# Performance work log

Measured on AMD Instinct MI355X. Metric: run time of the kernel, lower is better.

## Reference

```python
import jax, jax.numpy as jnp
import numpy as np


def _conv1x1_prelu(x, w, b, a):
    # 1x1 conv == channel matmul; PReLU with shared scalar slope a
    y = jnp.einsum('oc,nchw->nohw', w, x) + b[None, :, None, None]
    return jnp.where(y >= 0, y, a * y)


def setup_inputs() -> dict:
    key = jax.random.key(0)
    ks = jax.random.split(key, 7)
    N, C, H, W = 2, 128, 96, 96
    Ce = 64  # channel // reduction
    s_in = 1.0 / np.sqrt(C)
    return {
        'input': jax.random.normal(ks[0], (N, C, H, W), jnp.float32),
        'w1': jax.random.normal(ks[1], (Ce, C), jnp.float32) * s_in,
        'b1': jnp.zeros((Ce,), jnp.float32),
        'a1': jnp.full((1,), 0.25, jnp.float32),
        'w2': jax.random.normal(ks[2], (Ce, C), jnp.float32) * s_in,
        'b2': jnp.zeros((Ce,), jnp.float32),
        'a2': jnp.full((1,), 0.25, jnp.float32),
        'wa': jax.random.normal(ks[3], (C, C), jnp.float32) * s_in,
        'ba': jnp.zeros((C,), jnp.float32),
        'aa': jnp.full((1,), 0.25, jnp.float32),
    }


def reference(input, w1, b1, a1, w2, b2, a2, wa, ba, aa):
    e1 = _conv1x1_prelu(input, w1, b1, a1[0])  # [N, Ce, H, W]
    e2 = _conv1x1_prelu(input, w2, b2, a2[0])  # [N, Ce, H, W]
    xa = _conv1x1_prelu(input, wa, ba, aa[0])  # [N, C,  H, W]
    N, Ce, H, W = e1.shape
    HW = H * W
    q = e1.transpose(0, 2, 3, 1).reshape(N, HW, Ce)   # [N, HW, Ce]
    k = e2.reshape(N, Ce, HW)                          # [N, Ce, HW]
    score = jax.nn.softmax(jnp.matmul(q, k), axis=-1)  # [N, HW, HW] (no scale, as in source)
    v = xa.reshape(N, -1, HW).transpose(0, 2, 1)       # [N, HW, C]
    out = jnp.matmul(score, v)                         # [N, HW, C]
    return out.transpose(0, 2, 1).reshape(N, -1, H, W)
```

## Files before the change

### kernel.cpp

```cpp
#include <hip/hip_runtime.h>
#include <cstdint>
#include <cstddef>

#define HW_ 9216
#define CC 128
#define NQT 144
#define NQT2 72
#define LOG2E 1.44269504088896f

typedef short bf16x8 __attribute__((ext_vector_type(8)));
typedef unsigned short u16x4 __attribute__((ext_vector_type(4)));
typedef unsigned short u16x8 __attribute__((ext_vector_type(8)));
typedef float f32x4 __attribute__((ext_vector_type(4)));

__device__ __forceinline__ unsigned short f2bf(float f) {
    unsigned int u = __builtin_bit_cast(unsigned int, f);
    u += 0x7FFFu + ((u >> 16) & 1u);
    return (unsigned short)(u >> 16);
}

__device__ __forceinline__ float fast_exp2(float x) {
#if __has_builtin(__builtin_amdgcn_exp2f)
    return __builtin_amdgcn_exp2f(x);
#else
    return exp2f(x);
#endif
}

__device__ __forceinline__ unsigned int cvt_pk_bf16(float lo, float hi) {
    unsigned int r;
    asm("v_cvt_pk_bf16_f32 %0, %1, %2" : "=v"(r) : "v"(lo), "v"(hi));
    return r;
}

__global__ __launch_bounds__(256) void prep_w(const float* __restrict__ w1,
                                              const float* __restrict__ w2,
                                              const float* __restrict__ wa,
                                              float* __restrict__ wt) {
    int idx = blockIdx.x * 256 + threadIdx.x;
    int o = idx >> 7, c = idx & 127;
    float v;
    if (o < 64)       v = w1[o * 128 + c];
    else if (o < 128) v = w2[(o - 64) * 128 + c];
    else              v = wa[(o - 128) * 128 + c];
    wt[c * 256 + o] = v;
}

__global__ __launch_bounds__(256) void conv_kernel(
    const float* __restrict__ x, const float* __restrict__ wt,
    const float* __restrict__ b1, const float* __restrict__ a1,
    const float* __restrict__ b2, const float* __restrict__ a2,
    const float* __restrict__ ba, const float* __restrict__ aa,
    unsigned short* __restrict__ qb, unsigned short* __restrict__ kb,
    unsigned short* __restrict__ vtb) {
    const int ptile = blockIdx.x;
    const int oset  = blockIdx.y;
    const int n     = blockIdx.z;
    const int t = threadIdx.x;
    const int p = t & 63;
    const int og = __builtin_amdgcn_readfirstlane(t >> 6);
    const int p0 = ptile * 64;

    __shared__ float xs[128 * 64];
    for (int c = t >> 6; c < 128; c += 4)
        xs[c * 64 + p] = x[((size_t)n * CC + c) * HW_ + p0 + p];
    __syncthreads();

    const int obase = oset * 64 + og * 16;
    float acc[16];
#pragma unroll
    for (int i = 0; i < 16; i++) acc[i] = 0.f;

    for (int c = 0; c < 128; c++) {
        float xv = xs[c * 64 + p];
        const float* wr = wt + c * 256 + obase;
#pragma unroll
        for (int i = 0; i < 16; i++) acc[i] = fmaf(wr[i], xv, acc[i]);
    }

    const float* bias_p;
    const float* slope_p;
    if (oset == 0)      { bias_p = b1; slope_p = a1; }
    else if (oset == 1) { bias_p = b2; slope_p = a2; }
    else                { bias_p = ba; slope_p = aa; }
    const float slope = slope_p[0];

    unsigned short vals[16];
#pragma unroll
    for (int i = 0; i < 16; i++) {
        float bv = (oset < 2) ? bias_p[og * 16 + i] : bias_p[obase - 128 + i];
        float y = acc[i] + bv;
        y = (y >= 0.f) ? y : slope * y;
        if (oset == 0) y *= LOG2E;
        vals[i] = f2bf(y);
    }

    if (oset < 2) {
        unsigned short* dst = (oset == 0 ? qb : kb) + ((size_t)n * HW_ + p0 + p) * 64 + og * 16;
        bf16x8 v0, v1;
#pragma unroll
        for (int i = 0; i < 8; i++) { v0[i] = (short)vals[i]; v1[i] = (short)vals[8 + i]; }
        *(bf16x8*)(dst)     = v0;
        *(bf16x8*)(dst + 8) = v1;
    } else {
        int c0 = obase - 128;
#pragma unroll
        for (int i = 0; i < 16; i++)
            vtb[((size_t)n * CC + c0 + i) * HW_ + p0 + p] = vals[i];
    }
}

__global__ __launch_bounds__(256, 2) void attn_kernel(
    const unsigned short* __restrict__ qb, const unsigned short* __restrict__ kb,
    const unsigned short* __restrict__ vtb,
    float* __restrict__ o_part, float* __restrict__ l_part,
    int nch, int chunk_j) {
    const int qt    = blockIdx.x;
    const int chunk = blockIdx.y;
    const int n     = blockIdx.z;
    const int t = threadIdx.x;
    const int w = t >> 6;
    const int lane = t & 63;
    const int l15 = lane & 15;
    const int quad = lane >> 4;
    const int e7 = l15 & 7;

    __shared__ __align__(16) unsigned short k_lds[64 * 64];
    __shared__ __align__(16) unsigned short v_lds[128 * 64];
    __shared__ __align__(16) unsigned short p_lds[4 * 1024];

    const int row_ga = qt * 128 + w * 32 + l15;
    const int row_gb = row_ga + 16;
    const bf16x8 bq0a = *(const bf16x8*)(qb + ((size_t)n * HW_ + row_ga) * 64 + quad * 8);
    const bf16x8 bq1a = *(const bf16x8*)(qb + ((size_t)n * HW_ + row_ga) * 64 + 32 + quad * 8);
    const bf16x8 bq0b = *(const bf16x8*)(qb + ((size_t)n * HW_ + row_gb) * 64 + quad * 8);
    const bf16x8 bq1b = *(const bf16x8*)(qb + ((size_t)n * HW_ + row_gb) * 64 + 32 + quad * 8);

    f32x4 acc_oa[8], acc_ob[8];
#pragma unroll
    for (int i = 0; i < 8; i++) {
        acc_oa[i] = (f32x4){0.f, 0.f, 0.f, 0.f};
        acc_ob[i] = (f32x4){0.f, 0.f, 0.f, 0.f};
    }
    float l_sa = 0.f, l_sb = 0.f;

    const int stg_row = t >> 3, stg_seg = t & 7;
    const int iters = chunk_j / 64;
    int j0 = chunk * chunk_j;

    bf16x8 kr0, kr1, vr0, vr1, vr2, vr3;
    {
        const unsigned short* kp = kb + ((size_t)n * HW_ + j0 + stg_row) * 64 + stg_seg * 8;
        kr0 = *(const bf16x8*)kp;
        kr1 = *(const bf16x8*)(kp + 32 * 64);
        const unsigned short* vp = vtb + ((size_t)n * CC + stg_row) * HW_ + j0 + stg_seg * 8;
        vr0 = *(const bf16x8*)vp;
        vr1 = *(const bf16x8*)(vp + (size_t)32 * HW_);
        vr2 = *(const bf16x8*)(vp + (size_t)64 * HW_);
        vr3 = *(const bf16x8*)(vp + (size_t)96 * HW_);
    }

    for (int it = 0; it < iters; ++it, j0 += 64) {
        __syncthreads();
        {
            int r0 = stg_row, r1 = stg_row + 32;
            *(bf16x8*)&k_lds[r0 * 64 + ((stg_seg ^ (r0 & 7)) * 8)] = kr0;
            *(bf16x8*)&k_lds[r1 * 64 + ((stg_seg ^ (r1 & 7)) * 8)] = kr1;
            *(bf16x8*)&v_lds[r0 * 64 + ((stg_seg ^ (r0 & 7)) * 8)] = vr0;
            *(bf16x8*)&v_lds[r1 * 64 + ((stg_seg ^ (r1 & 7)) * 8)] = vr1;
            int r2 = stg_row + 64, r3 = stg_row + 96;
            *(bf16x8*)&v_lds[r2 * 64 + ((stg_seg ^ (r2 & 7)) * 8)] = vr2;
            *(bf16x8*)&v_lds[r3 * 64 + ((stg_seg ^ (r3 & 7)) * 8)] = vr3;
        }
        __syncthreads();

        if (it + 1 < iters) {
            const unsigned short* kp = kb + ((size_t)n * HW_ + j0 + 64 + stg_row) * 64 + stg_seg * 8;
            kr0 = *(const bf16x8*)kp;
            kr1 = *(const bf16x8*)(kp + 32 * 64);
            const unsigned short* vp = vtb + ((size_t)n * CC + stg_row) * HW_ + j0 + 64 + stg_seg * 8;
            vr0 = *(const bf16x8*)vp;
            vr1 = *(const bf16x8*)(vp + (size_t)32 * HW_);
            vr2 = *(const bf16x8*)(vp + (size_t)64 * HW_);
            vr3 = *(const bf16x8*)(vp + (size_t)96 * HW_);
        }

        f32x4 sa[4], sb[4];
#pragma unroll
        for (int ct = 0; ct < 4; ct++) {
            int jr = ct * 16 + l15;
            bf16x8 ak0 = *(const bf16x8*)&k_lds[jr * 64 + ((quad ^ e7) * 8)];
            bf16x8 ak1 = *(const bf16x8*)&k_lds[jr * 64 + (((4 + quad) ^ e7) * 8)];
            f32x4 za = (f32x4){0.f, 0.f, 0.f, 0.f};
            za = __builtin_amdgcn_mfma_f32_16x16x32_bf16(ak0, bq0a, za, 0, 0, 0);
            za = __builtin_amdgcn_mfma_f32_16x16x32_bf16(ak1, bq1a, za, 0, 0, 0);
            sa[ct] = za;
            f32x4 zb = (f32x4){0.f, 0.f, 0.f, 0.f};
            zb = __builtin_amdgcn_mfma_f32_16x16x32_bf16(ak0, bq0b, zb, 0, 0, 0);
            zb = __builtin_amdgcn_mfma_f32_16x16x32_bf16(ak1, bq1b, zb, 0, 0, 0);
            sb[ct] = zb;
        }

#pragma unroll
        for (int ct = 0; ct < 4; ct++) {
            sa[ct][0] = fast_exp2(sa[ct][0]);
            sa[ct][1] = fast_exp2(sa[ct][1]);
            sa[ct][2] = fast_exp2(sa[ct][2]);
            sa[ct][3] = fast_exp2(sa[ct][3]);
        }
        {
            float u0 = sa[0][0] + sa[0][1], u1 = sa[0][2] + sa[0][3];
            float u2 = sa[1][0] + sa[1][1], u3 = sa[1][2] + sa[1][3];
            float u4 = sa[2][0] + sa[2][1], u5 = sa[2][2] + sa[2][3];
            float u6 = sa[3][0] + sa[3][1], u7 = sa[3][2] + sa[3][3];
            float v0 = u0 + u1, v1 = u2 + u3, v2 = u4 + u5, v3 = u6 + u7;
            l_sa += (v0 + v1) + (v2 + v3);
        }
#pragma unroll
        for (int ct = 0; ct < 4; ct++) {
            unsigned int pk01 = cvt_pk_bf16(sa[ct][0], sa[ct][1]);
            unsigned int pk23 = cvt_pk_bf16(sa[ct][2], sa[ct][3]);
            int chunkid = 2 * ct + (quad >> 1);
            int off = l15 * 64 + ((chunkid ^ e7) * 8) + 4 * (quad & 1);
            uint2 tmp;
            tmp.x = pk01;
            tmp.y = pk23;
            *(u16x4*)&p_lds[w * 1024 + off] = __builtin_bit_cast(u16x4, tmp);
        }
        asm volatile("" ::: "memory");
        const bf16x8 bp0a = __builtin_bit_cast(bf16x8,
            *(const u16x8*)&p_lds[w * 1024 + l15 * 64 + ((quad ^ e7) * 8)]);
        const bf16x8 bp1a = __builtin_bit_cast(bf16x8,
            *(const u16x8*)&p_lds[w * 1024 + l15 * 64 + (((4 + quad) ^ e7) * 8)]);
        asm volatile("" ::: "memory");

#pragma unroll
        for (int ct = 0; ct < 4; ct++) {
            sb[ct][0] = fast_exp2(sb[ct][0]);
            sb[ct][1] = fast_exp2(sb[ct][1]);
            sb[ct][2] = fast_exp2(sb[ct][2]);
            sb[ct][3] = fast_exp2(sb[ct][3]);
        }
        {
            float u0 = sb[0][0] + sb[0][1], u1 = sb[0][2] + sb[0][3];
            float u2 = sb[1][0] + sb[1][1], u3 = sb[1][2] + sb[1][3];
            float u4 = sb[2][0] + sb[2][1], u5 = sb[2][2] + sb[2][3];
            float u6 = sb[3][0] + sb[3][1], u7 = sb[3][2] + sb[3][3];
            float v0 = u0 + u1, v1 = u2 + u3, v2 = u4 + u5, v3 = u6 + u7;
            l_sb += (v0 + v1) + (v2 + v3);
        }
#pragma unroll
        for (int ct = 0; ct < 4; ct++) {
            unsigned int pk01 = cvt_pk_bf16(sb[ct][0], sb[ct][1]);
            unsigned int pk23 = cvt_pk_bf16(sb[ct][2], sb[ct][3]);
            int chunkid = 2 * ct + (quad >> 1);
            int off = l15 * 64 + ((chunkid ^ e7) * 8) + 4 * (quad & 1);
            uint2 tmp;
            tmp.x = pk01;
            tmp.y = pk23;
            *(u16x4*)&p_lds[w * 1024 + off] = __builtin_bit_cast(u16x4, tmp);
        }
        asm volatile("" ::: "memory");
        const bf16x8 bp0b = __builtin_bit_cast(bf16x8,
            *(const u16x8*)&p_lds[w * 1024 + l15 * 64 + ((quad ^ e7) * 8)]);
        const bf16x8 bp1b = __builtin_bit_cast(bf16x8,
            *(const u16x8*)&p_lds[w * 1024 + l15 * 64 + (((4 + quad) ^ e7) * 8)]);
        asm volatile("" ::: "memory");

        __builtin_amdgcn_s_setprio(1);
#pragma unroll
        for (int ctv = 0; ctv < 8; ctv++) {
            int cr = ctv * 16 + l15;
            bf16x8 av0 = *(const bf16x8*)&v_lds[cr * 64 + ((quad ^ e7) * 8)];
            bf16x8 av1 = *(const bf16x8*)&v_lds[cr * 64 + (((4 + quad) ^ e7) * 8)];
            acc_oa[ctv] = __builtin_amdgcn_mfma_f32_16x16x32_bf16(av0, bp0a, acc_oa[ctv], 0, 0, 0);
            acc_oa[ctv] = __builtin_amdgcn_mfma_f32_16x16x32_bf16(av1, bp1a, acc_oa[ctv], 0, 0, 0);
            acc_ob[ctv] = __builtin_amdgcn_mfma_f32_16x16x32_bf16(av0, bp0b, acc_ob[ctv], 0, 0, 0);
            acc_ob[ctv] = __builtin_amdgcn_mfma_f32_16x16x32_bf16(av1, bp1b, acc_ob[ctv], 0, 0, 0);
        }
        __builtin_amdgcn_s_setprio(0);
    }

    l_sa += __shfl_xor(l_sa, 16);
    l_sa += __shfl_xor(l_sa, 32);
    l_sb += __shfl_xor(l_sb, 16);
    l_sb += __shfl_xor(l_sb, 32);

    const size_t cbase = ((size_t)(n * NQT2 + qt) * nch + chunk) * 128;
    const int qla = w * 32 + l15, qlb = qla + 16;
#pragma unroll
    for (int ctv = 0; ctv < 8; ctv++)
#pragma unroll
        for (int r = 0; r < 4; r++) {
            int c = ctv * 16 + 4 * quad + r;
            o_part[(cbase + c) * 128 + qla] = acc_oa[ctv][r];
            o_part[(cbase + c) * 128 + qlb] = acc_ob[ctv][r];
        }
    if (quad == 0) {
        size_t lb = ((size_t)(n * NQT2 + qt) * nch + chunk) * 128;
        l_part[lb + qla] = l_sa;
        l_part[lb + qlb] = l_sb;
    }
}

__global__ __launch_bounds__(256) void combine_kernel(
    const float* __restrict__ o_part, const float* __restrict__ lp,
    float* __restrict__ out, int nch) {
    int gid = blockIdx.x * 256 + threadIdx.x;
    int r = gid & 127;
    int rest = gid >> 7;
    int c = rest & 127;
    int nqt = rest >> 7;
    int n = nqt / NQT2, qtp = nqt - n * NQT2;

    float num = 0.f, den = 0.f;
    for (int ch = 0; ch < nch; ch++) {
        num += o_part[(((size_t)nqt * nch + ch) * 128 + c) * 128 + r];
        den += lp[((size_t)nqt * nch + ch) * 128 + r];
    }
    out[((size_t)n * CC + c) * HW_ + qtp * 128 + r] = num / den;
}

extern "C" void kernel_launch(void* const* d_in, const int* in_sizes, int n_in,
                              void* d_out, int out_size, void* d_ws, size_t ws_size,
                              hipStream_t stream) {
    const float* x  = (const float*)d_in[0];
    const float* w1 = (const float*)d_in[1];
    const float* b1 = (const float*)d_in[2];
    const float* a1 = (const float*)d_in[3];
    const float* w2 = (const float*)d_in[4];
    const float* b2 = (const float*)d_in[5];
    const float* a2 = (const float*)d_in[6];
    const float* wa = (const float*)d_in[7];
    const float* ba = (const float*)d_in[8];
    const float* aa = (const float*)d_in[9];
    float* out = (float*)d_out;

    auto need = [](int nc) -> size_t {
        return 9568256ull + (size_t)nc * 9437184ull + (size_t)nc * 73728ull;
    };
    int nch;
    if (ws_size >= need(6))      nch = 6;
    else if (ws_size >= need(4)) nch = 4;
    else                         nch = 2;
    const int chunk_j = HW_ / nch;

    char* ws = (char*)d_ws;
    float*          wt     = (float*)(ws + 0);
    unsigned short* qb     = (unsigned short*)(ws + 131072);
    unsigned short* kb     = (unsigned short*)(ws + 2490368);
    unsigned short* vtb    = (unsigned short*)(ws + 4849664);
    float*          o_part = (float*)(ws + 9568256);
    float*          lpart  = (float*)(ws + 9568256 + (size_t)nch * 9437184);

    hipLaunchKernelGGL(prep_w, dim3(128), dim3(256), 0, stream, w1, w2, wa, wt);
    hipLaunchKernelGGL(conv_kernel, dim3(144, 4, 2), dim3(256), 0, stream,
                       x, wt, b1, a1, b2, a2, ba, aa, qb, kb, vtb);
    hipLaunchKernelGGL(attn_kernel, dim3(NQT2, nch, 2), dim3(256), 0, stream,
                       qb, kb, vtb, o_part, lpart, nch, chunk_j);
    hipLaunchKernelGGL(combine_kernel, dim3(2 * NQT2 * 128 * 128 / 256), dim3(256), 0, stream,
                       o_part, lpart, out, nch);
}
```

Measured before the change: 200.6 us.

## Shrink attention blocks to 64 query rows with 2 waves, move K/V prefetch later

The attention kernel now uses 128-thread blocks covering 64 query rows instead of 256 threads covering 128, which doubles the grid in the query dimension. Each thread stages twice as many K/V vectors, and the partial-output and combine indexing is adjusted to match. The next-tile global prefetch moves from right after the LDS barrier to after the first P write, which may overlap the loads with the exp work. Each K/V tile is now reused by only 64 queries, so LDS staging traffic per query doubles and register pressure rises from the extra staged vectors.

```diff
diff --git a/kernel.cpp b/kernel.cpp
--- a/kernel.cpp
+++ b/kernel.cpp
@@ -5,7 +5,6 @@
 #define HW_ 9216
 #define CC 128
 #define NQT 144
-#define NQT2 72
 #define LOG2E 1.44269504088896f
 
 typedef short bf16x8 __attribute__((ext_vector_type(8)));
@@ -110,7 +109,7 @@
     }
 }
 
-__global__ __launch_bounds__(256, 2) void attn_kernel(
+__global__ __launch_bounds__(128, 3) void attn_kernel(
     const unsigned short* __restrict__ qb, const unsigned short* __restrict__ kb,
     const unsigned short* __restrict__ vtb,
     float* __restrict__ o_part, float* __restrict__ l_part,
@@ -127,9 +126,9 @@
 
     __shared__ __align__(16) unsigned short k_lds[64 * 64];
     __shared__ __align__(16) unsigned short v_lds[128 * 64];
-    __shared__ __align__(16) unsigned short p_lds[4 * 1024];
-
-    const int row_ga = qt * 128 + w * 32 + l15;
+    __shared__ __align__(16) unsigned short p_lds[2 * 1024];
+
+    const int row_ga = qt * 64 + w * 32 + l15;
     const int row_gb = row_ga + 16;
     const bf16x8 bq0a = *(const bf16x8*)(qb + ((size_t)n * HW_ + row_ga) * 64 + quad * 8);
     const bf16x8 bq1a = *(const bf16x8*)(qb + ((size_t)n * HW_ + row_ga) * 64 + 32 + quad * 8);
@@ -144,46 +143,47 @@
     }
     float l_sa = 0.f, l_sb = 0.f;
 
-    const int stg_row = t >> 3, stg_seg = t & 7;
+    const int stg_row = t >> 3;
+    const int stg_seg = t & 7;
     const int iters = chunk_j / 64;
     int j0 = chunk * chunk_j;
 
-    bf16x8 kr0, kr1, vr0, vr1, vr2, vr3;
+    bf16x8 kr0, kr1, kr2, kr3, vr0, vr1, vr2, vr3, vr4, vr5, vr6, vr7;
     {
         const unsigned short* kp = kb + ((size_t)n * HW_ + j0 + stg_row) * 64 + stg_seg * 8;
         kr0 = *(const bf16x8*)kp;
-        kr1 = *(const bf16x8*)(kp + 32 * 64);
+        kr1 = *(const bf16x8*)(kp + 16 * 64);
+        kr2 = *(const bf16x8*)(kp + 32 * 64);
+        kr3 = *(const bf16x8*)(kp + 48 * 64);
         const unsigned short* vp = vtb + ((size_t)n * CC + stg_row) * HW_ + j0 + stg_seg * 8;
         vr0 = *(const bf16x8*)vp;
-        vr1 = *(const bf16x8*)(vp + (size_t)32 * HW_);
-        vr2 = *(const bf16x8*)(vp + (size_t)64 * HW_);
-        vr3 = *(const bf16x8*)(vp + (size_t)96 * HW_);
+        vr1 = *(const bf16x8*)(vp + (size_t)16 * HW_);
+        vr2 = *(const bf16x8*)(vp + (size_t)32 * HW_);
+        vr3 = *(const bf16x8*)(vp + (size_t)48 * HW_);
+        vr4 = *(const bf16x8*)(vp + (size_t)64 * HW_);
+        vr5 = *(const bf16x8*)(vp + (size_t)80 * HW_);
+        vr6 = *(const bf16x8*)(vp + (size_t)96 * HW_);
+        vr7 = *(const bf16x8*)(vp + (size_t)112 * HW_);
     }
 
     for (int it = 0; it < iters; ++it, j0 += 64) {
         __syncthreads();
         {
-            int r0 = stg_row, r1 = stg_row + 32;
-            *(bf16x8*)&k_lds[r0 * 64 + ((stg_seg ^ (r0 & 7)) * 8)] = kr0;
-            *(bf16x8*)&k_lds[r1 * 64 + ((stg_seg ^ (r1 & 7)) * 8)] = kr1;
-            *(bf16x8*)&v_lds[r0 * 64 + ((stg_seg ^ (r0 & 7)) * 8)] = vr0;
-            *(bf16x8*)&v_lds[r1 * 64 + ((stg_seg ^ (r1 & 7)) * 8)] = vr1;
-            int r2 = stg_row + 64, r3 = stg_row + 96;
-            *(bf16x8*)&v_lds[r2 * 64 + ((stg_seg ^ (r2 & 7)) * 8)] = vr2;
-            *(bf16x8*)&v_lds[r3 * 64 + ((stg_seg ^ (r3 & 7)) * 8)] = vr3;
+            const int sw = (stg_seg ^ (stg_row & 7)) * 8;
+            *(bf16x8*)&k_lds[(stg_row +  0) * 64 + sw] = kr0;
+            *(bf16x8*)&k_lds[(stg_row + 16) * 64 + sw] = kr1;
+            *(bf16x8*)&k_lds[(stg_row + 32) * 64 + sw] = kr2;
+            *(bf16x8*)&k_lds[(stg_row + 48) * 64 + sw] = kr3;
+            *(bf16x8*)&v_lds[(stg_row +  0) * 64 + sw] = vr0;
+            *(bf16x8*)&v_lds[(stg_row + 16) * 64 + sw] = vr1;
+            *(bf16x8*)&v_lds[(stg_row + 32) * 64 + sw] = vr2;
+            *(bf16x8*)&v_lds[(stg_row + 48) * 64 + sw] = vr3;
+            *(bf16x8*)&v_lds[(stg_row + 64) * 64 + sw] = vr4;
+            *(bf16x8*)&v_lds[(stg_row + 80) * 64 + sw] = vr5;
+            *(bf16x8*)&v_lds[(stg_row + 96) * 64 + sw] = vr6;
+            *(bf16x8*)&v_lds[(stg_row + 112) * 64 + sw] = vr7;
         }
         __syncthreads();
-
-        if (it + 1 < iters) {
-            const unsigned short* kp = kb + ((size_t)n * HW_ + j0 + 64 + stg_row) * 64 + stg_seg * 8;
-            kr0 = *(const bf16x8*)kp;
-            kr1 = *(const bf16x8*)(kp + 32 * 64);
-            const unsigned short* vp = vtb + ((size_t)n * CC + stg_row) * HW_ + j0 + 64 + stg_seg * 8;
-            vr0 = *(const bf16x8*)vp;
-            vr1 = *(const bf16x8*)(vp + (size_t)32 * HW_);
-            vr2 = *(const bf16x8*)(vp + (size_t)64 * HW_);
-            vr3 = *(const bf16x8*)(vp + (size_t)96 * HW_);
-        }
 
         f32x4 sa[4], sb[4];
 #pragma unroll
@@ -234,6 +234,23 @@
             *(const u16x8*)&p_lds[w * 1024 + l15 * 64 + (((4 + quad) ^ e7) * 8)]);
         asm volatile("" ::: "memory");
 
+        if (it + 1 < iters) {
+            const unsigned short* kp = kb + ((size_t)n * HW_ + j0 + 64 + stg_row) * 64 + stg_seg * 8;
+            kr0 = *(const bf16x8*)kp;
+            kr1 = *(const bf16x8*)(kp + 16 * 64);
+            kr2 = *(const bf16x8*)(kp + 32 * 64);
+            kr3 = *(const bf16x8*)(kp + 48 * 64);
+            const unsigned short* vp = vtb + ((size_t)n * CC + stg_row) * HW_ + j0 + 64 + stg_seg * 8;
+            vr0 = *(const bf16x8*)vp;
+            vr1 = *(const bf16x8*)(vp + (size_t)16 * HW_);
+            vr2 = *(const bf16x8*)(vp + (size_t)32 * HW_);
+            vr3 = *(const bf16x8*)(vp + (size_t)48 * HW_);
+            vr4 = *(const bf16x8*)(vp + (size_t)64 * HW_);
+            vr5 = *(const bf16x8*)(vp + (size_t)80 * HW_);
+            vr6 = *(const bf16x8*)(vp + (size_t)96 * HW_);
+            vr7 = *(const bf16x8*)(vp + (size_t)112 * HW_);
+        }
+
 #pragma unroll
         for (int ct = 0; ct < 4; ct++) {
             sb[ct][0] = fast_exp2(sb[ct][0]);
@@ -286,18 +303,18 @@
     l_sb += __shfl_xor(l_sb, 16);
     l_sb += __shfl_xor(l_sb, 32);
 
-    const size_t cbase = ((size_t)(n * NQT2 + qt) * nch + chunk) * 128;
+    const size_t cbase = ((size_t)(n * NQT + qt) * nch + chunk) * 128;
     const int qla = w * 32 + l15, qlb = qla + 16;
 #pragma unroll
     for (int ctv = 0; ctv < 8; ctv++)
 #pragma unroll
         for (int r = 0; r < 4; r++) {
             int c = ctv * 16 + 4 * quad + r;
-            o_part[(cbase + c) * 128 + qla] = acc_oa[ctv][r];
-            o_part[(cbase + c) * 128 + qlb] = acc_ob[ctv][r];
+            o_part[(cbase + c) * 64 + qla] = acc_oa[ctv][r];
+            o_part[(cbase + c) * 64 + qlb] = acc_ob[ctv][r];
         }
     if (quad == 0) {
-        size_t lb = ((size_t)(n * NQT2 + qt) * nch + chunk) * 128;
+        size_t lb = ((size_t)(n * NQT + qt) * nch + chunk) * 64;
         l_part[lb + qla] = l_sa;
         l_part[lb + qlb] = l_sb;
     }
@@ -307,18 +324,18 @@
     const float* __restrict__ o_part, const float* __restrict__ lp,
     float* __restrict__ out, int nch) {
     int gid = blockIdx.x * 256 + threadIdx.x;
-    int r = gid & 127;
-    int rest = gid >> 7;
+    int r = gid & 63;
+    int rest = gid >> 6;
     int c = rest & 127;
     int nqt = rest >> 7;
-    int n = nqt / NQT2, qtp = nqt - n * NQT2;
+    int n = nqt / NQT, qtp = nqt - n * NQT;
 
     float num = 0.f, den = 0.f;
     for (int ch = 0; ch < nch; ch++) {
-        num += o_part[(((size_t)nqt * nch + ch) * 128 + c) * 128 + r];
-        den += lp[((size_t)nqt * nch + ch) * 128 + r];
-    }
-    out[((size_t)n * CC + c) * HW_ + qtp * 128 + r] = num / den;
+        num += o_part[(((size_t)nqt * nch + ch) * 128 + c) * 64 + r];
+        den += lp[((size_t)nqt * nch + ch) * 64 + r];
+    }
+    out[((size_t)n * CC + c) * HW_ + qtp * 64 + r] = num / den;
 }
 
 extern "C" void kernel_launch(void* const* d_in, const int* in_sizes, int n_in,
@@ -356,8 +373,8 @@
     hipLaunchKernelGGL(prep_w, dim3(128), dim3(256), 0, stream, w1, w2, wa, wt);
     hipLaunchKernelGGL(conv_kernel, dim3(144, 4, 2), dim3(256), 0, stream,
                        x, wt, b1, a1, b2, a2, ba, aa, qb, kb, vtb);
-    hipLaunchKernelGGL(attn_kernel, dim3(NQT2, nch, 2), dim3(256), 0, stream,
+    hipLaunchKernelGGL(attn_kernel, dim3(NQT, nch, 2), dim3(128), 0, stream,
                        qb, kb, vtb, o_part, lpart, nch, chunk_j);
-    hipLaunchKernelGGL(combine_kernel, dim3(2 * NQT2 * 128 * 128 / 256), dim3(256), 0, stream,
+    hipLaunchKernelGGL(combine_kernel, dim3(2 * NQT * 128 * 64 / 256), dim3(256), 0, stream,
                        o_part, lpart, out, nch);
 }
```

Result: slower. 374.8 us (+86.8%).

## Replace LDS-staged K/V tiles with direct global loads in single-wave blocks

Applied to the files above, without the earlier changes.

The attention kernel now runs one 64-thread wave per block covering 32 query rows, instead of four waves sharing K and V tiles staged through LDS. Each wave loads its K and V MFMA operands straight from global memory, which removes both block barriers and the LDS staging. The grid grows to 288 query tiles, and the partial-output layout and the combine kernel are re-indexed to match. The cost is that K/V reuse across waves now depends on the cache hierarchy rather than LDS, so global and L2 traffic may rise sharply and the loads become less coalesced.

```diff
diff --git a/kernel.cpp b/kernel.cpp
--- a/kernel.cpp
+++ b/kernel.cpp
@@ -5,7 +5,7 @@
 #define HW_ 9216
 #define CC 128
 #define NQT 144
-#define NQT2 72
+#define NQT3 288
 #define LOG2E 1.44269504088896f
 
 typedef short bf16x8 __attribute__((ext_vector_type(8)));
@@ -110,7 +110,7 @@
     }
 }
 
-__global__ __launch_bounds__(256, 2) void attn_kernel(
+__global__ __launch_bounds__(64, 3) void attn_kernel(
     const unsigned short* __restrict__ qb, const unsigned short* __restrict__ kb,
     const unsigned short* __restrict__ vtb,
     float* __restrict__ o_part, float* __restrict__ l_part,
@@ -118,18 +118,14 @@
     const int qt    = blockIdx.x;
     const int chunk = blockIdx.y;
     const int n     = blockIdx.z;
-    const int t = threadIdx.x;
-    const int w = t >> 6;
-    const int lane = t & 63;
+    const int lane = threadIdx.x;
     const int l15 = lane & 15;
     const int quad = lane >> 4;
     const int e7 = l15 & 7;
 
-    __shared__ __align__(16) unsigned short k_lds[64 * 64];
-    __shared__ __align__(16) unsigned short v_lds[128 * 64];
-    __shared__ __align__(16) unsigned short p_lds[4 * 1024];
-
-    const int row_ga = qt * 128 + w * 32 + l15;
+    __shared__ __align__(16) unsigned short p_lds[1024];
+
+    const int row_ga = qt * 32 + l15;
     const int row_gb = row_ga + 16;
     const bf16x8 bq0a = *(const bf16x8*)(qb + ((size_t)n * HW_ + row_ga) * 64 + quad * 8);
     const bf16x8 bq1a = *(const bf16x8*)(qb + ((size_t)n * HW_ + row_ga) * 64 + 32 + quad * 8);
@@ -144,53 +140,19 @@
     }
     float l_sa = 0.f, l_sb = 0.f;
 
-    const int stg_row = t >> 3, stg_seg = t & 7;
+    const unsigned short* kbase = kb + ((size_t)n * HW_) * 64 + (l15 * 64) + quad * 8;
+    const unsigned short* vbase = vtb + ((size_t)n * CC + l15) * HW_ + quad * 8;
+
     const int iters = chunk_j / 64;
     int j0 = chunk * chunk_j;
 
-    bf16x8 kr0, kr1, vr0, vr1, vr2, vr3;
-    {
-        const unsigned short* kp = kb + ((size_t)n * HW_ + j0 + stg_row) * 64 + stg_seg * 8;
-        kr0 = *(const bf16x8*)kp;
-        kr1 = *(const bf16x8*)(kp + 32 * 64);
-        const unsigned short* vp = vtb + ((size_t)n * CC + stg_row) * HW_ + j0 + stg_seg * 8;
-        vr0 = *(const bf16x8*)vp;
-        vr1 = *(const bf16x8*)(vp + (size_t)32 * HW_);
-        vr2 = *(const bf16x8*)(vp + (size_t)64 * HW_);
-        vr3 = *(const bf16x8*)(vp + (size_t)96 * HW_);
-    }
-
     for (int it = 0; it < iters; ++it, j0 += 64) {
-        __syncthreads();
-        {
-            int r0 = stg_row, r1 = stg_row + 32;
-            *(bf16x8*)&k_lds[r0 * 64 + ((stg_seg ^ (r0 & 7)) * 8)] = kr0;
-            *(bf16x8*)&k_lds[r1 * 64 + ((stg_seg ^ (r1 & 7)) * 8)] = kr1;
-            *(bf16x8*)&v_lds[r0 * 64 + ((stg_seg ^ (r0 & 7)) * 8)] = vr0;
-            *(bf16x8*)&v_lds[r1 * 64 + ((stg_seg ^ (r1 & 7)) * 8)] = vr1;
-            int r2 = stg_row + 64, r3 = stg_row + 96;
-            *(bf16x8*)&v_lds[r2 * 64 + ((stg_seg ^ (r2 & 7)) * 8)] = vr2;
-            *(bf16x8*)&v_lds[r3 * 64 + ((stg_seg ^ (r3 & 7)) * 8)] = vr3;
-        }
-        __syncthreads();
-
-        if (it + 1 < iters) {
-            const unsigned short* kp = kb + ((size_t)n * HW_ + j0 + 64 + stg_row) * 64 + stg_seg * 8;
-            kr0 = *(const bf16x8*)kp;
-            kr1 = *(const bf16x8*)(kp + 32 * 64);
-            const unsigned short* vp = vtb + ((size_t)n * CC + stg_row) * HW_ + j0 + 64 + stg_seg * 8;
-            vr0 = *(const bf16x8*)vp;
-            vr1 = *(const bf16x8*)(vp + (size_t)32 * HW_);
-            vr2 = *(const bf16x8*)(vp + (size_t)64 * HW_);
-            vr3 = *(const bf16x8*)(vp + (size_t)96 * HW_);
-        }
-
         f32x4 sa[4], sb[4];
 #pragma unroll
         for (int ct = 0; ct < 4; ct++) {
-            int jr = ct * 16 + l15;
-            bf16x8 ak0 = *(const bf16x8*)&k_lds[jr * 64 + ((quad ^ e7) * 8)];
-            bf16x8 ak1 = *(const bf16x8*)&k_lds[jr * 64 + (((4 + quad) ^ e7) * 8)];
+            const unsigned short* kp = kbase + (size_t)(j0 + ct * 16) * 64;
+            bf16x8 ak0 = *(const bf16x8*)kp;
+            bf16x8 ak1 = *(const bf16x8*)(kp + 32);
             f32x4 za = (f32x4){0.f, 0.f, 0.f, 0.f};
             za = __builtin_amdgcn_mfma_f32_16x16x32_bf16(ak0, bq0a, za, 0, 0, 0);
             za = __builtin_amdgcn_mfma_f32_16x16x32_bf16(ak1, bq1a, za, 0, 0, 0);
@@ -225,13 +187,13 @@
             uint2 tmp;
             tmp.x = pk01;
             tmp.y = pk23;
-            *(u16x4*)&p_lds[w * 1024 + off] = __builtin_bit_cast(u16x4, tmp);
+            *(u16x4*)&p_lds[off] = __builtin_bit_cast(u16x4, tmp);
         }
         asm volatile("" ::: "memory");
         const bf16x8 bp0a = __builtin_bit_cast(bf16x8,
-            *(const u16x8*)&p_lds[w * 1024 + l15 * 64 + ((quad ^ e7) * 8)]);
+            *(const u16x8*)&p_lds[l15 * 64 + ((quad ^ e7) * 8)]);
         const bf16x8 bp1a = __builtin_bit_cast(bf16x8,
-            *(const u16x8*)&p_lds[w * 1024 + l15 * 64 + (((4 + quad) ^ e7) * 8)]);
+            *(const u16x8*)&p_lds[l15 * 64 + (((4 + quad) ^ e7) * 8)]);
         asm volatile("" ::: "memory");
 
 #pragma unroll
@@ -258,21 +220,21 @@
             uint2 tmp;
             tmp.x = pk01;
             tmp.y = pk23;
-            *(u16x4*)&p_lds[w * 1024 + off] = __builtin_bit_cast(u16x4, tmp);
+            *(u16x4*)&p_lds[off] = __builtin_bit_cast(u16x4, tmp);
         }
         asm volatile("" ::: "memory");
         const bf16x8 bp0b = __builtin_bit_cast(bf16x8,
-            *(const u16x8*)&p_lds[w * 1024 + l15 * 64 + ((quad ^ e7) * 8)]);
+            *(const u16x8*)&p_lds[l15 * 64 + ((quad ^ e7) * 8)]);
         const bf16x8 bp1b = __builtin_bit_cast(bf16x8,
-            *(const u16x8*)&p_lds[w * 1024 + l15 * 64 + (((4 + quad) ^ e7) * 8)]);
+            *(const u16x8*)&p_lds[l15 * 64 + (((4 + quad) ^ e7) * 8)]);
         asm volatile("" ::: "memory");
 
         __builtin_amdgcn_s_setprio(1);
 #pragma unroll
         for (int ctv = 0; ctv < 8; ctv++) {
-            int cr = ctv * 16 + l15;
-            bf16x8 av0 = *(const bf16x8*)&v_lds[cr * 64 + ((quad ^ e7) * 8)];
-            bf16x8 av1 = *(const bf16x8*)&v_lds[cr * 64 + (((4 + quad) ^ e7) * 8)];
+            const unsigned short* vp = vbase + (size_t)(ctv * 16) * HW_ + j0;
+            bf16x8 av0 = *(const bf16x8*)vp;
+            bf16x8 av1 = *(const bf16x8*)(vp + 32);
             acc_oa[ctv] = __builtin_amdgcn_mfma_f32_16x16x32_bf16(av0, bp0a, acc_oa[ctv], 0, 0, 0);
             acc_oa[ctv] = __builtin_amdgcn_mfma_f32_16x16x32_bf16(av1, bp1a, acc_oa[ctv], 0, 0, 0);
             acc_ob[ctv] = __builtin_amdgcn_mfma_f32_16x16x32_bf16(av0, bp0b, acc_ob[ctv], 0, 0, 0);
@@ -286,18 +248,18 @@
     l_sb += __shfl_xor(l_sb, 16);
     l_sb += __shfl_xor(l_sb, 32);
 
-    const size_t cbase = ((size_t)(n * NQT2 + qt) * nch + chunk) * 128;
-    const int qla = w * 32 + l15, qlb = qla + 16;
+    const size_t cbase = ((size_t)(n * NQT3 + qt) * nch + chunk) * 128;
+    const int qla = l15, qlb = 16 + l15;
 #pragma unroll
     for (int ctv = 0; ctv < 8; ctv++)
 #pragma unroll
         for (int r = 0; r < 4; r++) {
             int c = ctv * 16 + 4 * quad + r;
-            o_part[(cbase + c) * 128 + qla] = acc_oa[ctv][r];
-            o_part[(cbase + c) * 128 + qlb] = acc_ob[ctv][r];
+            o_part[(cbase + c) * 32 + qla] = acc_oa[ctv][r];
+            o_part[(cbase + c) * 32 + qlb] = acc_ob[ctv][r];
         }
     if (quad == 0) {
-        size_t lb = ((size_t)(n * NQT2 + qt) * nch + chunk) * 128;
+        size_t lb = ((size_t)(n * NQT3 + qt) * nch + chunk) * 32;
         l_part[lb + qla] = l_sa;
         l_part[lb + qlb] = l_sb;
     }
@@ -307,18 +269,18 @@
     const float* __restrict__ o_part, const float* __restrict__ lp,
     float* __restrict__ out, int nch) {
     int gid = blockIdx.x * 256 + threadIdx.x;
-    int r = gid & 127;
-    int rest = gid >> 7;
+    int r = gid & 31;
+    int rest = gid >> 5;
     int c = rest & 127;
     int nqt = rest >> 7;
-    int n = nqt / NQT2, qtp = nqt - n * NQT2;
+    int n = nqt / NQT3, qtp = nqt - n * NQT3;
 
     float num = 0.f, den = 0.f;
     for (int ch = 0; ch < nch; ch++) {
-        num += o_part[(((size_t)nqt * nch + ch) * 128 + c) * 128 + r];
-        den += lp[((size_t)nqt * nch + ch) * 128 + r];
-    }
-    out[((size_t)n * CC + c) * HW_ + qtp * 128 + r] = num / den;
+        num += o_part[(((size_t)nqt * nch + ch) * 128 + c) * 32 + r];
+        den += lp[((size_t)nqt * nch + ch) * 32 + r];
+    }
+    out[((size_t)n * CC + c) * HW_ + qtp * 32 + r] = num / den;
 }
 
 extern "C" void kernel_launch(void* const* d_in, const int* in_sizes, int n_in,
@@ -356,8 +318,8 @@
     hipLaunchKernelGGL(prep_w, dim3(128), dim3(256), 0, stream, w1, w2, wa, wt);
     hipLaunchKernelGGL(conv_kernel, dim3(144, 4, 2), dim3(256), 0, stream,
                        x, wt, b1, a1, b2, a2, ba, aa, qb, kb, vtb);
-    hipLaunchKernelGGL(attn_kernel, dim3(NQT2, nch, 2), dim3(256), 0, stream,
+    hipLaunchKernelGGL(attn_kernel, dim3(NQT3, nch, 2), dim3(64), 0, stream,
                        qb, kb, vtb, o_part, lpart, nch, chunk_j);
-    hipLaunchKernelGGL(combine_kernel, dim3(2 * NQT2 * 128 * 128 / 256), dim3(256), 0, stream,
+    hipLaunchKernelGGL(combine_kernel, dim3(2 * NQT3 * 128 * 32 / 256), dim3(256), 0, stream,
                        o_part, lpart, out, nch);
 }
```

New measurement: 390.5 us. +94.6%, slower.
